# Optimization experiments

Measured on AMD Instinct MI355X. Metric: run time of the kernel, lower is better.

## Reference

```python
import jax, jax.numpy as jnp
import numpy as np

N_HEAD = 16
EPS = 1e-6


def setup_inputs() -> dict:
    key = jax.random.key(0)
    k1, k2, k3 = jax.random.split(key, 3)
    B, T, C = 2, 2048, 1024
    x = jax.random.normal(k1, (B, T, C), dtype=jnp.float32)
    w_attn = jax.random.normal(k2, (C, 3 * C), dtype=jnp.float32) * 0.02
    w_proj = jax.random.normal(k3, (C, C), dtype=jnp.float32) * 0.02
    return {"x": x, "w_attn": w_attn, "w_proj": w_proj}


def _linear_attention(q, k, v):
    """q,k,v: (T,B,H,D) with q,k already feature-mapped (elu+1).
    Causal linear attention via a D x D running-state recurrence (same math
    as cumsum of k-v outer products, computed without the O(T*D^2) tensor)."""
    B, H, D = q.shape[1], q.shape[2], q.shape[3]

    def step(carry, qkv_t):
        S, z = carry                      # S:(B,H,D,D), z:(B,H,D)
        qt, kt, vt = qkv_t                # each (B,H,D)
        S = S + kt[..., :, None] * vt[..., None, :]
        z = z + kt
        num = jnp.einsum('bhi,bhij->bhj', qt, S)
        den = jnp.sum(qt * z, axis=-1, keepdims=True)
        return (S, z), num / (den + EPS)

    S0 = jnp.zeros((B, H, D, D), q.dtype)
    z0 = jnp.zeros((B, H, D), q.dtype)
    _, y = jax.lax.scan(step, (S0, z0), (q, k, v))
    return y                              # (T,B,H,D)


def reference(x, w_attn, w_proj):
    B, T, C = x.shape
    H = N_HEAD
    D = C // H
    qkv = x @ w_attn                      # (B,T,3C)
    q, k, v = jnp.split(qkv, 3, axis=-1)

    def to_tbhd(a):                       # (B,T,C) -> (T,B,H,D)
        return a.reshape(B, T, H, D).transpose(1, 0, 2, 3)

    q = jax.nn.elu(to_tbhd(q)) + 1.0      # phi(x) = ELU(x)+1
    k = jax.nn.elu(to_tbhd(k)) + 1.0
    v = to_tbhd(v)

    y = _linear_attention(q, k, v)        # (T,B,H,D)
    y = y.transpose(1, 0, 2, 3).reshape(B, T, C)
    return y @ w_proj                     # resid dropout p=0.0 is identity
```

## Files before the change

kernel.cpp:

```cpp
#include <hip/hip_runtime.h>
#include <hip/hip_bf16.h>
#include <cmath>

#define TB   2048
#define CCH  1024
#define NCH  32
#define EPSF 1e-6f

typedef unsigned short u16;
typedef __attribute__((ext_vector_type(8))) short  frag8;
typedef __attribute__((ext_vector_type(4))) float  floatx4;

__device__ __forceinline__ u16 f2bf(float f) {
    unsigned int u = __float_as_uint(f);
    unsigned int r = (u + 0x7fffu + ((u >> 16) & 1u)) >> 16;
    return (u16)r;
}
__device__ __forceinline__ float bf2f(u16 v) {
    return __uint_as_float(((unsigned int)v) << 16);
}

__device__ __forceinline__ void async_load16(const u16* g, u16* l) {
    __builtin_amdgcn_global_load_lds(
        (const __attribute__((address_space(1))) void*)g,
        (__attribute__((address_space(3))) void*)l,
        16, 0, 0);
}

__global__ __launch_bounds__(256) void prep_k(
    const float* __restrict__ x, const float* __restrict__ wa,
    const float* __restrict__ wp,
    u16* __restrict__ xb, u16* __restrict__ waT, u16* __restrict__ wpT)
{
    __shared__ u16 t[64][72];
    int blk = blockIdx.x;
    if (blk < 2048) {
        int i = (blk * 256 + threadIdx.x) * 8;
        float4 a = *(const float4*)(x + i);
        float4 b = *(const float4*)(x + i + 4);
        u16 v[8];
        v[0] = f2bf(a.x); v[1] = f2bf(a.y); v[2] = f2bf(a.z); v[3] = f2bf(a.w);
        v[4] = f2bf(b.x); v[5] = f2bf(b.y); v[6] = f2bf(b.z); v[7] = f2bf(b.w);
        *(uint4*)(xb + i) = *(uint4*)v;
        return;
    }
    const float* in; u16* out; int K, N, bx, by;
    if (blk < 2048 + 768) {
        int tb = blk - 2048; in = wa; out = waT; K = 1024; N = 3072;
        bx = tb % 48; by = tb / 48;
    } else {
        int tb = blk - 2816; in = wp; out = wpT; K = 1024; N = 1024;
        bx = tb & 15; by = tb >> 4;
    }
    const int k0 = by * 64, n0 = bx * 64;
    #pragma unroll
    for (int i = 0; i < 4; ++i) {
        int rr = (threadIdx.x >> 4) + 16 * i;
        int c4 = (threadIdx.x & 15) * 4;
        float4 v = *(const float4*)(in + (size_t)(k0 + rr) * N + n0 + c4);
        t[c4 + 0][rr] = f2bf(v.x);
        t[c4 + 1][rr] = f2bf(v.y);
        t[c4 + 2][rr] = f2bf(v.z);
        t[c4 + 3][rr] = f2bf(v.w);
    }
    __syncthreads();
    #pragma unroll
    for (int i = 0; i < 2; ++i) {
        int rr = (threadIdx.x >> 3) + 32 * i;
        int c8 = (threadIdx.x & 7) * 8;
        u16 o[8];
        #pragma unroll
        for (int q = 0; q < 8; ++q) o[q] = t[rr][c8 + q];
        *(uint4*)(out + (size_t)(n0 + rr) * K + k0 + c8) = *(uint4*)o;
    }
}

__global__ __launch_bounds__(256, 2) void gemm1_k(
    const u16* __restrict__ A, const u16* __restrict__ BT,
    u16* __restrict__ C, int N, int K, int phi_cols)
{
    __shared__ u16 Als[2][128 * 64];
    __shared__ u16 Bls[2][192 * 64];
    const int tid  = threadIdx.x;
    const int wave = tid >> 6, lane = tid & 63;
    const int quad = lane >> 4, lrow = lane & 15;
    const int wm = wave >> 1, wn = wave & 1;
    const int row0 = blockIdx.y * 128, col0 = blockIdx.x * 192;
    const int lr = lane >> 3;
    const int lc = ((lane & 7) ^ lr) * 8;
    const int rsw = lrow & 7;
    floatx4 acc[4][6] = {};
    const int NT = K >> 6;

    #pragma unroll
    for (int m = 0; m < 4; ++m) {
        int i = wave * 4 + m;
        async_load16(A + (size_t)(row0 + i * 8 + lr) * K + lc, &Als[0][i * 512]);
    }
    #pragma unroll
    for (int m = 0; m < 6; ++m) {
        int i = wave * 6 + m;
        async_load16(BT + (size_t)(col0 + i * 8 + lr) * K + lc, &Bls[0][i * 512]);
    }

    for (int t = 0; t < NT; ++t) {
        const int p = t & 1;
        if (t + 1 < NT) {
            const int k0 = (t + 1) << 6;
            #pragma unroll
            for (int m = 0; m < 4; ++m) {
                int i = wave * 4 + m;
                async_load16(A + (size_t)(row0 + i * 8 + lr) * K + k0 + lc,
                             &Als[p ^ 1][i * 512]);
            }
            #pragma unroll
            for (int m = 0; m < 6; ++m) {
                int i = wave * 6 + m;
                async_load16(BT + (size_t)(col0 + i * 8 + lr) * K + k0 + lc,
                             &Bls[p ^ 1][i * 512]);
            }
            __builtin_amdgcn_sched_barrier(0);
            asm volatile("s_waitcnt vmcnt(10)" ::: "memory");
        } else {
            asm volatile("s_waitcnt vmcnt(0)" ::: "memory");
        }
        __builtin_amdgcn_s_barrier();
        __builtin_amdgcn_sched_barrier(0);

        #pragma unroll
        for (int ksi = 0; ksi < 2; ++ksi) {
            frag8 af[4], bf[6];
            #pragma unroll
            for (int i = 0; i < 4; ++i)
                af[i] = *(const frag8*)&Als[p][(wm * 64 + i * 16 + lrow) * 64
                                              + ((ksi * 4 + quad) ^ rsw) * 8];
            #pragma unroll
            for (int j = 0; j < 6; ++j)
                bf[j] = *(const frag8*)&Bls[p][(wn * 96 + j * 16 + lrow) * 64
                                              + ((ksi * 4 + quad) ^ rsw) * 8];
            #pragma unroll
            for (int i = 0; i < 4; ++i)
                #pragma unroll
                for (int j = 0; j < 6; ++j)
                    acc[i][j] = __builtin_amdgcn_mfma_f32_16x16x32_bf16(
                        af[i], bf[j], acc[i][j], 0, 0, 0);
        }

        asm volatile("s_waitcnt lgkmcnt(0)" ::: "memory");
        __builtin_amdgcn_sched_barrier(0);
        __builtin_amdgcn_s_barrier();
    }

    #pragma unroll
    for (int i = 0; i < 4; ++i) {
        #pragma unroll
        for (int j = 0; j < 6; ++j) {
            int col = col0 + wn * 96 + j * 16 + lrow;
            bool isphi = col < phi_cols;
            #pragma unroll
            for (int r = 0; r < 4; ++r) {
                int row = row0 + wm * 64 + i * 16 + quad * 4 + r;
                float v = acc[i][j][r];
                if (isphi) v = (v > 0.f) ? (v + 1.f) : __expf(v);
                C[(size_t)row * N + col] = f2bf(v);
            }
        }
    }
}

__global__ __launch_bounds__(256, 2) void gemm_bf16_f32out_k(
    const u16* __restrict__ A, const u16* __restrict__ BT,
    float* __restrict__ C, int N, int K)
{
    __shared__ u16 Als[2][128 * 64];
    __shared__ u16 Bls[2][64 * 64];
    const int tid  = threadIdx.x;
    const int wave = tid >> 6, lane = tid & 63;
    const int quad = lane >> 4, lrow = lane & 15;
    const int wm = wave >> 1, wn = wave & 1;
    const int row0 = blockIdx.y * 128, col0 = blockIdx.x * 64;
    const int lr = lane >> 3;
    const int lc = ((lane & 7) ^ lr) * 8;
    const int rsw = lrow & 7;
    floatx4 acc[4][2] = {};
    const int NT = K >> 6;

    #pragma unroll
    for (int m = 0; m < 4; ++m) {
        int i = wave * 4 + m;
        async_load16(A + (size_t)(row0 + i * 8 + lr) * K + lc, &Als[0][i * 512]);
    }
    #pragma unroll
    for (int m = 0; m < 2; ++m) {
        int i = wave * 2 + m;
        async_load16(BT + (size_t)(col0 + i * 8 + lr) * K + lc, &Bls[0][i * 512]);
    }

    for (int t = 0; t < NT; ++t) {
        const int p = t & 1;
        if (t + 1 < NT) {
            const int k0 = (t + 1) << 6;
            #pragma unroll
            for (int m = 0; m < 4; ++m) {
                int i = wave * 4 + m;
                async_load16(A + (size_t)(row0 + i * 8 + lr) * K + k0 + lc,
                             &Als[p ^ 1][i * 512]);
            }
            #pragma unroll
            for (int m = 0; m < 2; ++m) {
                int i = wave * 2 + m;
                async_load16(BT + (size_t)(col0 + i * 8 + lr) * K + k0 + lc,
                             &Bls[p ^ 1][i * 512]);
            }
            __builtin_amdgcn_sched_barrier(0);
            asm volatile("s_waitcnt vmcnt(6)" ::: "memory");
        } else {
            asm volatile("s_waitcnt vmcnt(0)" ::: "memory");
        }
        __builtin_amdgcn_s_barrier();
        __builtin_amdgcn_sched_barrier(0);

        #pragma unroll
        for (int ksi = 0; ksi < 2; ++ksi) {
            frag8 af[4], bf[2];
            #pragma unroll
            for (int i = 0; i < 4; ++i)
                af[i] = *(const frag8*)&Als[p][(wm * 64 + i * 16 + lrow) * 64
                                              + ((ksi * 4 + quad) ^ rsw) * 8];
            #pragma unroll
            for (int jn = 0; jn < 2; ++jn)
                bf[jn] = *(const frag8*)&Bls[p][(wn * 32 + jn * 16 + lrow) * 64
                                               + ((ksi * 4 + quad) ^ rsw) * 8];
            #pragma unroll
            for (int i = 0; i < 4; ++i)
                #pragma unroll
                for (int jn = 0; jn < 2; ++jn)
                    acc[i][jn] = __builtin_amdgcn_mfma_f32_16x16x32_bf16(
                        af[i], bf[jn], acc[i][jn], 0, 0, 0);
        }

        asm volatile("s_waitcnt lgkmcnt(0)" ::: "memory");
        __builtin_amdgcn_sched_barrier(0);
        __builtin_amdgcn_s_barrier();
    }

    #pragma unroll
    for (int i = 0; i < 4; ++i)
        #pragma unroll
        for (int jn = 0; jn < 2; ++jn) {
            int col = col0 + wn * 32 + jn * 16 + lrow;
            #pragma unroll
            for (int r = 0; r < 4; ++r) {
                int row = row0 + wm * 64 + i * 16 + quad * 4 + r;
                C[(size_t)row * N + col] = acc[i][jn][r];
            }
        }
}

__global__ __launch_bounds__(256) void chunk_kv_mfma_k(
    const u16* __restrict__ qkv,
    u16* __restrict__ Spt,
    float* __restrict__ zloc,
    u16* __restrict__ VtG)
{
    __shared__ u16 Kt[64][72];
    __shared__ u16 Vt[64][72];
    const int tid  = threadIdx.x;
    const int wave = tid >> 6, lane = tid & 63;
    const int quad = lane >> 4, lrow = lane & 15;
    const int blk = blockIdx.x;
    const int c = blk & 31, h = (blk >> 5) & 15, b = blk >> 9;
    const int t0 = c * 64;
    const u16* base = qkv + (size_t)(b * TB + t0) * 3072 + h * 64;

    #pragma unroll
    for (int m = 0; m < 2; ++m) {
        int chunk = tid + 256 * m;
        int s = chunk >> 3, d0 = (chunk & 7) * 8;
        const u16* row = base + (size_t)s * 3072;
        u16 kv[8], vv[8];
        *(uint4*)kv = *(const uint4*)(row + 1024 + d0);
        *(uint4*)vv = *(const uint4*)(row + 2048 + d0);
        #pragma unroll
        for (int q = 0; q < 8; ++q) { Kt[d0 + q][s] = kv[q]; Vt[d0 + q][s] = vv[q]; }
    }
    __syncthreads();

    #pragma unroll
    for (int m = 0; m < 2; ++m) {
        int e = tid + 256 * m;
        int r = e >> 3, c8 = (e & 7) * 8;
        u16 o[8];
        #pragma unroll
        for (int q = 0; q < 8; ++q) o[q] = Vt[r][c8 + q];
        *(uint4*)(VtG + (size_t)blk * 4096 + r * 64 + c8) = *(uint4*)o;
    }

    frag8 vf[2];
    #pragma unroll
    for (int ks = 0; ks < 2; ++ks)
        vf[ks] = *(const frag8*)&Vt[wave * 16 + lrow][ks * 32 + quad * 8];
    u16* So = Spt + (size_t)blk * 4096;
    #pragma unroll
    for (int jn = 0; jn < 4; ++jn) {
        floatx4 acc = {};
        #pragma unroll
        for (int ks = 0; ks < 2; ++ks) {
            frag8 kf = *(const frag8*)&Kt[jn * 16 + lrow][ks * 32 + quad * 8];
            acc = __builtin_amdgcn_mfma_f32_16x16x32_bf16(vf[ks], kf, acc, 0, 0, 0);
        }
        #pragma unroll
        for (int r = 0; r < 4; ++r) {
            int j = wave * 16 + quad * 4 + r;
            int i = jn * 16 + lrow;
            So[j * 64 + i] = f2bf(acc[r]);
        }
    }
    if (tid < 64) {
        float z = 0.f;
        for (int s = 0; s < 64; ++s) z += bf2f(Kt[tid][s]);
        zloc[(size_t)blk * 64 + tid] = z;
    }
}

__global__ __launch_bounds__(256) void scan_state_k(
    u16* __restrict__ Spt, float* __restrict__ z)
{
    const int bh = blockIdx.x >> 2;
    const int part = blockIdx.x & 3;
    const int e0 = part * 1024 + threadIdx.x * 4;
    const size_t base = (size_t)bh * NCH * 4096;
    float r[4] = {};
    for (int c = 0; c < NCH; ++c) {
        u16* p = Spt + base + (size_t)c * 4096 + e0;
        u16 t[4];
        *(uint2*)t = *(const uint2*)p;
        u16 o[4];
        #pragma unroll
        for (int q = 0; q < 4; ++q) { o[q] = f2bf(r[q]); r[q] += bf2f(t[q]); }
        *(uint2*)p = *(uint2*)o;
    }
    if (part == 0 && threadIdx.x < 64) {
        const size_t zb = (size_t)bh * NCH * 64;
        float rz = 0.f;
        for (int c = 0; c < NCH; ++c) {
            float t = z[zb + c * 64 + threadIdx.x];
            z[zb + c * 64 + threadIdx.x] = rz;
            rz += t;
        }
    }
}

__global__ __launch_bounds__(256) void attn_mfma_k(
    const u16* __restrict__ qkv,
    const u16* __restrict__ SptG,
    const float* __restrict__ zp,
    const u16* __restrict__ VtG,
    u16* __restrict__ Yb)
{
    __shared__ u16 Qls[64 * 64];
    __shared__ u16 Kls[64 * 64];
    __shared__ u16 Vls[64 * 64];
    __shared__ u16 Sls[64 * 64];
    __shared__ float zps[64];
    __shared__ float den4[64][4];
    __shared__ float den[64];

    const int tid  = threadIdx.x;
    const int wave = tid >> 6, lane = tid & 63;
    const int quad = lane >> 4, lrow = lane & 15;
    const int blk = blockIdx.x;
    const int c = blk & 31, h = (blk >> 5) & 15, b = blk >> 9;
    const int t0 = c * 64;
    const int lr = lane >> 3;
    const int lc = ((lane & 7) ^ lr) * 8;
    const int rsw = lrow & 7;
    const u16* qbase = qkv + (size_t)(b * TB + t0) * 3072 + h * 64;

    #pragma unroll
    for (int m = 0; m < 2; ++m) {
        int i = wave * 2 + m;
        int r = i * 8 + lr;
        async_load16(qbase + (size_t)r * 3072 + lc,          &Qls[i * 512]);
        async_load16(qbase + (size_t)r * 3072 + 1024 + lc,   &Kls[i * 512]);
        async_load16(SptG + (size_t)blk * 4096 + r * 64 + lc, &Sls[i * 512]);
        async_load16(VtG  + (size_t)blk * 4096 + r * 64 + lc, &Vls[i * 512]);
    }
    if (tid < 64) zps[tid] = zp[(size_t)blk * 64 + tid];
    __syncthreads();

    frag8 qf[2];
    #pragma unroll
    for (int ks = 0; ks < 2; ++ks)
        qf[ks] = *(const frag8*)&Qls[(wave * 16 + lrow) * 64 + ((ks * 4 + quad) ^ rsw) * 8];

    floatx4 yacc[4] = {}, kacc[4] = {};
    #pragma unroll
    for (int jn = 0; jn < 4; ++jn) {
        #pragma unroll
        for (int ks = 0; ks < 2; ++ks) {
            frag8 spf = *(const frag8*)&Sls[(jn * 16 + lrow) * 64 + ((ks * 4 + quad) ^ rsw) * 8];
            yacc[jn] = __builtin_amdgcn_mfma_f32_16x16x32_bf16(qf[ks], spf, yacc[jn], 0, 0, 0);
            frag8 kf = *(const frag8*)&Kls[(jn * 16 + lrow) * 64 + ((ks * 4 + quad) ^ rsw) * 8];
            kacc[jn] = __builtin_amdgcn_mfma_f32_16x16x32_bf16(qf[ks], kf, kacc[jn], 0, 0, 0);
        }
    }
    __syncthreads();

    #pragma unroll
    for (int jn = 0; jn < 4; ++jn) {
        int s = jn * 16 + lrow;
        #pragma unroll
        for (int r = 0; r < 4; ++r) {
            int t = wave * 16 + quad * 4 + r;
            float v = (s <= t) ? kacc[jn][r] : 0.f;
            Sls[t * 64 + (((s >> 3) ^ (t & 7)) * 8) + (s & 7)] = f2bf(v);
        }
    }
    __syncthreads();

    {
        int t = tid >> 2, seg = tid & 3;
        float p = 0.f;
        #pragma unroll
        for (int g2 = 0; g2 < 2; ++g2) {
            int g = seg * 2 + g2;
            int pq = ((g ^ (t & 7)) * 8);
            const u16* qp = &Qls[t * 64 + pq];
            const u16* ap = &Sls[t * 64 + pq];
            #pragma unroll
            for (int e = 0; e < 8; ++e) {
                p += bf2f(qp[e]) * zps[g * 8 + e] + bf2f(ap[e]);
            }
        }
        den4[t][seg] = p;
    }

    frag8 af2[2];
    #pragma unroll
    for (int ks = 0; ks < 2; ++ks)
        af2[ks] = *(const frag8*)&Sls[(wave * 16 + lrow) * 64 + ((ks * 4 + quad) ^ rsw) * 8];
    #pragma unroll
    for (int jn = 0; jn < 4; ++jn)
        #pragma unroll
        for (int ks = 0; ks < 2; ++ks) {
            frag8 vf = *(const frag8*)&Vls[(jn * 16 + lrow) * 64 + ((ks * 4 + quad) ^ rsw) * 8];
            yacc[jn] = __builtin_amdgcn_mfma_f32_16x16x32_bf16(af2[ks], vf, yacc[jn], 0, 0, 0);
        }
    __syncthreads();
    if (tid < 64) den[tid] = den4[tid][0] + den4[tid][1] + den4[tid][2] + den4[tid][3];
    __syncthreads();

    #pragma unroll
    for (int jn = 0; jn < 4; ++jn) {
        #pragma unroll
        for (int r = 0; r < 4; ++r) {
            int t = wave * 16 + quad * 4 + r;
            float inv = 1.f / (den[t] + EPSF);
            Qls[t * 64 + jn * 16 + lrow] = f2bf(yacc[jn][r] * inv);
        }
    }
    __syncthreads();
    {
        int row = tid >> 2, seg = tid & 3;
        size_t o = (size_t)(b * TB + t0 + row) * CCH + h * 64 + seg * 16;
        *(uint4*)(Yb + o)     = *(uint4*)&Qls[row * 64 + seg * 16];
        *(uint4*)(Yb + o + 8) = *(uint4*)&Qls[row * 64 + seg * 16 + 8];
    }
}

extern "C" void kernel_launch(void* const* d_in, const int* in_sizes, int n_in,
                              void* d_out, int out_size, void* d_ws, size_t ws_size,
                              hipStream_t stream)
{
    const float* x      = (const float*)d_in[0];
    const float* w_attn = (const float*)d_in[1];
    const float* w_proj = (const float*)d_in[2];
    float* out = (float*)d_out;

    u16* xb    = (u16*)d_ws;
    u16* waT   = xb    + (size_t)4096 * 1024;
    u16* wpT   = waT   + (size_t)3072 * 1024;
    u16* Yb    = wpT   + (size_t)1024 * 1024;
    u16* qkv_b = Yb    + (size_t)4096 * 1024;
    u16* Spt   = qkv_b + (size_t)4096 * 3072;
    u16* VtG   = Spt   + (size_t)1024 * 4096;
    float* zloc = (float*)(VtG + (size_t)1024 * 4096);

    prep_k<<<3072, 256, 0, stream>>>(x, w_attn, w_proj, xb, waT, wpT);

    gemm1_k<<<dim3(16, 32), 256, 0, stream>>>(xb, waT, qkv_b, 3072, 1024, 2048);

    chunk_kv_mfma_k<<<1024, 256, 0, stream>>>(qkv_b, Spt, zloc, VtG);
    scan_state_k   <<<128,  256, 0, stream>>>(Spt, zloc);
    attn_mfma_k    <<<1024, 256, 0, stream>>>(qkv_b, Spt, zloc, VtG, Yb);

    gemm_bf16_f32out_k<<<dim3(16, 32), 256, 0, stream>>>(Yb, wpT, out, 1024, 1024);
}
```

Baseline: 154.7 us.

## Fuse chunk state, scan and attention into one sequential per-head kernel

Replaces the three-kernel chunked linear attention (per-chunk KV state, a global prefix scan, then per-chunk attention) with one kernel where each block owns a (batch, head) pair and walks its 32 chunks in order. The running state and z sum stay in registers and LDS, and the next chunk's Q/K/V are prefetched into registers while the current one computes. This removes the global round trips for the state, VtG and z buffers and two launches. In exchange only 32 blocks run on a GPU with far more compute units, and each block's work is serial across chunks.

```diff
diff --git a/kernel.cpp b/kernel.cpp
--- a/kernel.cpp
+++ b/kernel.cpp
@@ -257,215 +257,203 @@
         }
 }
 
-__global__ __launch_bounds__(256) void chunk_kv_mfma_k(
-    const u16* __restrict__ qkv,
-    u16* __restrict__ Spt,
-    float* __restrict__ zloc,
-    u16* __restrict__ VtG)
+__global__ __launch_bounds__(256) void fused_attn_k(
+    const u16* __restrict__ qkv, u16* __restrict__ Yb)
 {
-    __shared__ u16 Kt[64][72];
-    __shared__ u16 Vt[64][72];
+    __shared__ u16 Qls[64 * 64];
+    __shared__ u16 Kls[64 * 64];
+    __shared__ u16 Kt[64 * 72];
+    __shared__ u16 Vt[64 * 72];
+    __shared__ u16 As[64 * 64];
+    __shared__ u16 Spb[64 * 64];
+    __shared__ float zps[64];
+    __shared__ float den4[64][4];
+
     const int tid  = threadIdx.x;
     const int wave = tid >> 6, lane = tid & 63;
     const int quad = lane >> 4, lrow = lane & 15;
-    const int blk = blockIdx.x;
-    const int c = blk & 31, h = (blk >> 5) & 15, b = blk >> 9;
-    const int t0 = c * 64;
-    const u16* base = qkv + (size_t)(b * TB + t0) * 3072 + h * 64;
-
-    #pragma unroll
-    for (int m = 0; m < 2; ++m) {
-        int chunk = tid + 256 * m;
-        int s = chunk >> 3, d0 = (chunk & 7) * 8;
-        const u16* row = base + (size_t)s * 3072;
-        u16 kv[8], vv[8];
-        *(uint4*)kv = *(const uint4*)(row + 1024 + d0);
-        *(uint4*)vv = *(const uint4*)(row + 2048 + d0);
-        #pragma unroll
-        for (int q = 0; q < 8; ++q) { Kt[d0 + q][s] = kv[q]; Vt[d0 + q][s] = vv[q]; }
-    }
-    __syncthreads();
-
-    #pragma unroll
-    for (int m = 0; m < 2; ++m) {
-        int e = tid + 256 * m;
-        int r = e >> 3, c8 = (e & 7) * 8;
-        u16 o[8];
-        #pragma unroll
-        for (int q = 0; q < 8; ++q) o[q] = Vt[r][c8 + q];
-        *(uint4*)(VtG + (size_t)blk * 4096 + r * 64 + c8) = *(uint4*)o;
-    }
-
-    frag8 vf[2];
-    #pragma unroll
-    for (int ks = 0; ks < 2; ++ks)
-        vf[ks] = *(const frag8*)&Vt[wave * 16 + lrow][ks * 32 + quad * 8];
-    u16* So = Spt + (size_t)blk * 4096;
-    #pragma unroll
-    for (int jn = 0; jn < 4; ++jn) {
-        floatx4 acc = {};
-        #pragma unroll
-        for (int ks = 0; ks < 2; ++ks) {
-            frag8 kf = *(const frag8*)&Kt[jn * 16 + lrow][ks * 32 + quad * 8];
-            acc = __builtin_amdgcn_mfma_f32_16x16x32_bf16(vf[ks], kf, acc, 0, 0, 0);
-        }
-        #pragma unroll
-        for (int r = 0; r < 4; ++r) {
-            int j = wave * 16 + quad * 4 + r;
-            int i = jn * 16 + lrow;
-            So[j * 64 + i] = f2bf(acc[r]);
-        }
-    }
-    if (tid < 64) {
-        float z = 0.f;
-        for (int s = 0; s < 64; ++s) z += bf2f(Kt[tid][s]);
-        zloc[(size_t)blk * 64 + tid] = z;
-    }
-}
-
-__global__ __launch_bounds__(256) void scan_state_k(
-    u16* __restrict__ Spt, float* __restrict__ z)
-{
-    const int bh = blockIdx.x >> 2;
-    const int part = blockIdx.x & 3;
-    const int e0 = part * 1024 + threadIdx.x * 4;
-    const size_t base = (size_t)bh * NCH * 4096;
-    float r[4] = {};
-    for (int c = 0; c < NCH; ++c) {
-        u16* p = Spt + base + (size_t)c * 4096 + e0;
-        u16 t[4];
-        *(uint2*)t = *(const uint2*)p;
-        u16 o[4];
-        #pragma unroll
-        for (int q = 0; q < 4; ++q) { o[q] = f2bf(r[q]); r[q] += bf2f(t[q]); }
-        *(uint2*)p = *(uint2*)o;
-    }
-    if (part == 0 && threadIdx.x < 64) {
-        const size_t zb = (size_t)bh * NCH * 64;
-        float rz = 0.f;
-        for (int c = 0; c < NCH; ++c) {
-            float t = z[zb + c * 64 + threadIdx.x];
-            z[zb + c * 64 + threadIdx.x] = rz;
-            rz += t;
-        }
-    }
-}
-
-__global__ __launch_bounds__(256) void attn_mfma_k(
-    const u16* __restrict__ qkv,
-    const u16* __restrict__ SptG,
-    const float* __restrict__ zp,
-    const u16* __restrict__ VtG,
-    u16* __restrict__ Yb)
-{
-    __shared__ u16 Qls[64 * 64];
-    __shared__ u16 Kls[64 * 64];
-    __shared__ u16 Vls[64 * 64];
-    __shared__ u16 Sls[64 * 64];
-    __shared__ float zps[64];
-    __shared__ float den4[64][4];
-    __shared__ float den[64];
-
-    const int tid  = threadIdx.x;
-    const int wave = tid >> 6, lane = tid & 63;
-    const int quad = lane >> 4, lrow = lane & 15;
-    const int blk = blockIdx.x;
-    const int c = blk & 31, h = (blk >> 5) & 15, b = blk >> 9;
-    const int t0 = c * 64;
     const int lr = lane >> 3;
     const int lc = ((lane & 7) ^ lr) * 8;
     const int rsw = lrow & 7;
-    const u16* qbase = qkv + (size_t)(b * TB + t0) * 3072 + h * 64;
-
-    #pragma unroll
-    for (int m = 0; m < 2; ++m) {
-        int i = wave * 2 + m;
-        int r = i * 8 + lr;
-        async_load16(qbase + (size_t)r * 3072 + lc,          &Qls[i * 512]);
-        async_load16(qbase + (size_t)r * 3072 + 1024 + lc,   &Kls[i * 512]);
-        async_load16(SptG + (size_t)blk * 4096 + r * 64 + lc, &Sls[i * 512]);
-        async_load16(VtG  + (size_t)blk * 4096 + r * 64 + lc, &Vls[i * 512]);
-    }
-    if (tid < 64) zps[tid] = zp[(size_t)blk * 64 + tid];
-    __syncthreads();
-
-    frag8 qf[2];
-    #pragma unroll
-    for (int ks = 0; ks < 2; ++ks)
-        qf[ks] = *(const frag8*)&Qls[(wave * 16 + lrow) * 64 + ((ks * 4 + quad) ^ rsw) * 8];
-
-    floatx4 yacc[4] = {}, kacc[4] = {};
-    #pragma unroll
-    for (int jn = 0; jn < 4; ++jn) {
-        #pragma unroll
-        for (int ks = 0; ks < 2; ++ks) {
-            frag8 spf = *(const frag8*)&Sls[(jn * 16 + lrow) * 64 + ((ks * 4 + quad) ^ rsw) * 8];
-            yacc[jn] = __builtin_amdgcn_mfma_f32_16x16x32_bf16(qf[ks], spf, yacc[jn], 0, 0, 0);
-            frag8 kf = *(const frag8*)&Kls[(jn * 16 + lrow) * 64 + ((ks * 4 + quad) ^ rsw) * 8];
-            kacc[jn] = __builtin_amdgcn_mfma_f32_16x16x32_bf16(qf[ks], kf, kacc[jn], 0, 0, 0);
-        }
-    }
-    __syncthreads();
-
-    #pragma unroll
-    for (int jn = 0; jn < 4; ++jn) {
-        int s = jn * 16 + lrow;
-        #pragma unroll
-        for (int r = 0; r < 4; ++r) {
-            int t = wave * 16 + quad * 4 + r;
-            float v = (s <= t) ? kacc[jn][r] : 0.f;
-            Sls[t * 64 + (((s >> 3) ^ (t & 7)) * 8) + (s & 7)] = f2bf(v);
-        }
-    }
-    __syncthreads();
+    const int bh = blockIdx.x;
+    const int b = bh >> 4, h = bh & 15;
+    const u16* base = qkv + (size_t)b * TB * 3072 + h * 64;
 
     {
-        int t = tid >> 2, seg = tid & 3;
-        float p = 0.f;
-        #pragma unroll
-        for (int g2 = 0; g2 < 2; ++g2) {
-            int g = seg * 2 + g2;
-            int pq = ((g ^ (t & 7)) * 8);
-            const u16* qp = &Qls[t * 64 + pq];
-            const u16* ap = &Sls[t * 64 + pq];
-            #pragma unroll
-            for (int e = 0; e < 8; ++e) {
-                p += bf2f(qp[e]) * zps[g * 8 + e] + bf2f(ap[e]);
-            }
-        }
-        den4[t][seg] = p;
-    }
-
-    frag8 af2[2];
-    #pragma unroll
-    for (int ks = 0; ks < 2; ++ks)
-        af2[ks] = *(const frag8*)&Sls[(wave * 16 + lrow) * 64 + ((ks * 4 + quad) ^ rsw) * 8];
-    #pragma unroll
-    for (int jn = 0; jn < 4; ++jn)
-        #pragma unroll
-        for (int ks = 0; ks < 2; ++ks) {
-            frag8 vf = *(const frag8*)&Vls[(jn * 16 + lrow) * 64 + ((ks * 4 + quad) ^ rsw) * 8];
-            yacc[jn] = __builtin_amdgcn_mfma_f32_16x16x32_bf16(af2[ks], vf, yacc[jn], 0, 0, 0);
-        }
-    __syncthreads();
-    if (tid < 64) den[tid] = den4[tid][0] + den4[tid][1] + den4[tid][2] + den4[tid][3];
-    __syncthreads();
-
-    #pragma unroll
-    for (int jn = 0; jn < 4; ++jn) {
-        #pragma unroll
-        for (int r = 0; r < 4; ++r) {
-            int t = wave * 16 + quad * 4 + r;
-            float inv = 1.f / (den[t] + EPSF);
-            Qls[t * 64 + jn * 16 + lrow] = f2bf(yacc[jn][r] * inv);
-        }
-    }
-    __syncthreads();
+        uint4 z4 = {0, 0, 0, 0};
+        *(uint4*)&Spb[tid * 16]     = z4;
+        *(uint4*)&Spb[tid * 16 + 8] = z4;
+        if (tid < 64) zps[tid] = 0.f;
+    }
+    floatx4 spf[4] = {};
+
+    uint4 qst[2], kst[2], ktr[2], vtr[2];
+    const int sp = tid >> 3, d0t = (tid & 7) * 8, s0 = sp * 2;
+
     {
-        int row = tid >> 2, seg = tid & 3;
-        size_t o = (size_t)(b * TB + t0 + row) * CCH + h * 64 + seg * 16;
-        *(uint4*)(Yb + o)     = *(uint4*)&Qls[row * 64 + seg * 16];
-        *(uint4*)(Yb + o + 8) = *(uint4*)&Qls[row * 64 + seg * 16 + 8];
+        const u16* cb = base;
+        #pragma unroll
+        for (int m = 0; m < 2; ++m) {
+            int r = (wave * 2 + m) * 8 + lr;
+            qst[m] = *(const uint4*)(cb + (size_t)r * 3072 + lc);
+            kst[m] = *(const uint4*)(cb + (size_t)r * 3072 + 1024 + lc);
+        }
+        ktr[0] = *(const uint4*)(cb + (size_t)s0 * 3072 + 1024 + d0t);
+        ktr[1] = *(const uint4*)(cb + (size_t)(s0 + 1) * 3072 + 1024 + d0t);
+        vtr[0] = *(const uint4*)(cb + (size_t)s0 * 3072 + 2048 + d0t);
+        vtr[1] = *(const uint4*)(cb + (size_t)(s0 + 1) * 3072 + 2048 + d0t);
+    }
+
+    for (int c = 0; c < NCH; ++c) {
+        #pragma unroll
+        for (int m = 0; m < 2; ++m) {
+            int i = wave * 2 + m;
+            *(uint4*)&Qls[i * 512 + lane * 8] = qst[m];
+            *(uint4*)&Kls[i * 512 + lane * 8] = kst[m];
+        }
+        {
+            const u16* k0p = (const u16*)&ktr[0]; const u16* k1p = (const u16*)&ktr[1];
+            const u16* v0p = (const u16*)&vtr[0]; const u16* v1p = (const u16*)&vtr[1];
+            #pragma unroll
+            for (int q = 0; q < 8; ++q) {
+                unsigned kw = (unsigned)k0p[q] | ((unsigned)k1p[q] << 16);
+                unsigned vw = (unsigned)v0p[q] | ((unsigned)v1p[q] << 16);
+                *(unsigned*)&Kt[(d0t + q) * 72 + s0] = kw;
+                *(unsigned*)&Vt[(d0t + q) * 72 + s0] = vw;
+            }
+        }
+        __syncthreads();
+
+        if (c + 1 < NCH) {
+            const u16* cb = base + (size_t)(c + 1) * 64 * 3072;
+            #pragma unroll
+            for (int m = 0; m < 2; ++m) {
+                int r = (wave * 2 + m) * 8 + lr;
+                qst[m] = *(const uint4*)(cb + (size_t)r * 3072 + lc);
+                kst[m] = *(const uint4*)(cb + (size_t)r * 3072 + 1024 + lc);
+            }
+            ktr[0] = *(const uint4*)(cb + (size_t)s0 * 3072 + 1024 + d0t);
+            ktr[1] = *(const uint4*)(cb + (size_t)(s0 + 1) * 3072 + 1024 + d0t);
+            vtr[0] = *(const uint4*)(cb + (size_t)s0 * 3072 + 2048 + d0t);
+            vtr[1] = *(const uint4*)(cb + (size_t)(s0 + 1) * 3072 + 2048 + d0t);
+            __builtin_amdgcn_sched_barrier(0);
+        }
+
+        frag8 qf[2];
+        #pragma unroll
+        for (int ks = 0; ks < 2; ++ks)
+            qf[ks] = *(const frag8*)&Qls[(wave * 16 + lrow) * 64 + ((ks * 4 + quad) ^ rsw) * 8];
+
+        floatx4 yacc[4] = {}, kacc[4] = {};
+        #pragma unroll
+        for (int jn = 0; jn < 4; ++jn) {
+            #pragma unroll
+            for (int ks = 0; ks < 2; ++ks) {
+                frag8 spf8 = *(const frag8*)&Spb[(jn * 16 + lrow) * 64 + ((ks * 4 + quad) ^ rsw) * 8];
+                yacc[jn] = __builtin_amdgcn_mfma_f32_16x16x32_bf16(qf[ks], spf8, yacc[jn], 0, 0, 0);
+                frag8 kf = *(const frag8*)&Kls[(jn * 16 + lrow) * 64 + ((ks * 4 + quad) ^ rsw) * 8];
+                kacc[jn] = __builtin_amdgcn_mfma_f32_16x16x32_bf16(qf[ks], kf, kacc[jn], 0, 0, 0);
+            }
+        }
+        #pragma unroll
+        for (int jn = 0; jn < 4; ++jn) {
+            int s = jn * 16 + lrow;
+            #pragma unroll
+            for (int r = 0; r < 4; ++r) {
+                int t = wave * 16 + quad * 4 + r;
+                float v = (s <= t) ? kacc[jn][r] : 0.f;
+                As[t * 64 + (((s >> 3) ^ (t & 7)) * 8) + (s & 7)] = f2bf(v);
+            }
+        }
+        __syncthreads();
+
+        {
+            int t = tid >> 2, seg = tid & 3;
+            float p = 0.f;
+            #pragma unroll
+            for (int g2 = 0; g2 < 2; ++g2) {
+                int g = seg * 2 + g2;
+                int pq = ((g ^ (t & 7)) * 8);
+                const u16* qp = &Qls[t * 64 + pq];
+                const u16* ap = &As[t * 64 + pq];
+                #pragma unroll
+                for (int e = 0; e < 8; ++e)
+                    p += bf2f(qp[e]) * zps[g * 8 + e] + bf2f(ap[e]);
+            }
+            den4[t][seg] = p;
+        }
+        {
+            frag8 af2[2];
+            #pragma unroll
+            for (int ks = 0; ks < 2; ++ks)
+                af2[ks] = *(const frag8*)&As[(wave * 16 + lrow) * 64 + ((ks * 4 + quad) ^ rsw) * 8];
+            #pragma unroll
+            for (int jn = 0; jn < 4; ++jn)
+                #pragma unroll
+                for (int ks = 0; ks < 2; ++ks) {
+                    frag8 vf = *(const frag8*)&Vt[(jn * 16 + lrow) * 72 + ks * 32 + quad * 8];
+                    yacc[jn] = __builtin_amdgcn_mfma_f32_16x16x32_bf16(af2[ks], vf, yacc[jn], 0, 0, 0);
+                }
+        }
+        __syncthreads();
+
+        {
+            frag8 vf2[2];
+            #pragma unroll
+            for (int ks = 0; ks < 2; ++ks)
+                vf2[ks] = *(const frag8*)&Vt[(wave * 16 + lrow) * 72 + ks * 32 + quad * 8];
+            #pragma unroll
+            for (int jn = 0; jn < 4; ++jn) {
+                floatx4 sc = {};
+                #pragma unroll
+                for (int ks = 0; ks < 2; ++ks) {
+                    frag8 kf2 = *(const frag8*)&Kt[(jn * 16 + lrow) * 72 + ks * 32 + quad * 8];
+                    sc = __builtin_amdgcn_mfma_f32_16x16x32_bf16(vf2[ks], kf2, sc, 0, 0, 0);
+                }
+                spf[jn] += sc;
+                int i = jn * 16 + lrow;
+                #pragma unroll
+                for (int r = 0; r < 4; ++r) {
+                    int j = wave * 16 + quad * 4 + r;
+                    Spb[j * 64 + (((i >> 3) ^ (j & 7)) * 8) + (i & 7)] = f2bf(spf[jn][r]);
+                }
+            }
+        }
+        if (tid < 64) {
+            float zc = 0.f;
+            #pragma unroll
+            for (int g = 0; g < 8; ++g) {
+                u16 kk[8];
+                *(uint4*)kk = *(const uint4*)&Kt[tid * 72 + g * 8];
+                #pragma unroll
+                for (int e = 0; e < 8; ++e) zc += bf2f(kk[e]);
+            }
+            zps[tid] += zc;
+        }
+        {
+            float inv[4];
+            #pragma unroll
+            for (int r = 0; r < 4; ++r) {
+                int t = wave * 16 + quad * 4 + r;
+                float d = den4[t][0] + den4[t][1] + den4[t][2] + den4[t][3];
+                inv[r] = 1.f / (d + EPSF);
+            }
+            #pragma unroll
+            for (int jn = 0; jn < 4; ++jn)
+                #pragma unroll
+                for (int r = 0; r < 4; ++r) {
+                    int t = wave * 16 + quad * 4 + r;
+                    As[t * 64 + jn * 16 + lrow] = f2bf(yacc[jn][r] * inv[r]);
+                }
+        }
+        __syncthreads();
+
+        {
+            int row = tid >> 2, seg = tid & 3;
+            size_t o = (size_t)(b * TB + c * 64 + row) * CCH + h * 64 + seg * 16;
+            *(uint4*)(Yb + o)     = *(uint4*)&As[row * 64 + seg * 16];
+            *(uint4*)(Yb + o + 8) = *(uint4*)&As[row * 64 + seg * 16 + 8];
+        }
     }
 }
 
@@ -483,17 +471,12 @@
     u16* wpT   = waT   + (size_t)3072 * 1024;
     u16* Yb    = wpT   + (size_t)1024 * 1024;
     u16* qkv_b = Yb    + (size_t)4096 * 1024;
-    u16* Spt   = qkv_b + (size_t)4096 * 3072;
-    u16* VtG   = Spt   + (size_t)1024 * 4096;
-    float* zloc = (float*)(VtG + (size_t)1024 * 4096);
 
     prep_k<<<3072, 256, 0, stream>>>(x, w_attn, w_proj, xb, waT, wpT);
 
     gemm1_k<<<dim3(16, 32), 256, 0, stream>>>(xb, waT, qkv_b, 3072, 1024, 2048);
 
-    chunk_kv_mfma_k<<<1024, 256, 0, stream>>>(qkv_b, Spt, zloc, VtG);
-    scan_state_k   <<<128,  256, 0, stream>>>(Spt, zloc);
-    attn_mfma_k    <<<1024, 256, 0, stream>>>(qkv_b, Spt, zloc, VtG, Yb);
+    fused_attn_k<<<32, 256, 0, stream>>>(qkv_b, Yb);
 
     gemm_bf16_f32out_k<<<dim3(16, 32), 256, 0, stream>>>(Yb, wpT, out, 1024, 1024);
 }
```

After: 245.8 us. +58.9%, slower.
